# Optimization experiments

Hardware: AMD Instinct MI355X
Metric: run time of the kernel (lower is better)

The kernel has to match this reference:

```python
import jax, jax.numpy as jnp
import numpy as np

D_MODEL = 2048
N_HEADS = 32
N_KV_HEADS = 8
ROPE_BASE = 10000.0


def setup_inputs() -> dict:
    key = jax.random.key(0)
    ks = jax.random.split(key, 5)
    b, s, d = 2, 2048, D_MODEL
    hd = d // N_HEADS
    scale = 0.02
    return {
        "x": jax.random.normal(ks[0], (b, s, d), jnp.float32),
        "wq": jax.random.normal(ks[1], (N_HEADS * hd, d), jnp.float32) * scale,
        "wk": jax.random.normal(ks[2], (N_KV_HEADS * hd, d), jnp.float32) * scale,
        "wv": jax.random.normal(ks[3], (N_KV_HEADS * hd, d), jnp.float32) * scale,
        "wo": jax.random.normal(ks[4], (d, N_HEADS * hd), jnp.float32) * scale,
    }


def _rope_cos_sin(seq_len, head_dim):
    # theta_j = base^(-2j/d); freqs[i, j] = i * theta_j; repeat-interleave x2 on last dim
    theta = 1.0 / (ROPE_BASE ** (jnp.arange(0, head_dim, 2, dtype=jnp.float32) / head_dim))
    freqs = jnp.arange(seq_len, dtype=jnp.float32)[:, None] * theta[None, :]  # [S, hd/2]
    cos = jnp.repeat(jnp.cos(freqs), 2, axis=-1)[None, :, None, :]  # [1, S, 1, hd]
    sin = jnp.repeat(jnp.sin(freqs), 2, axis=-1)[None, :, None, :]
    return cos, sin


def _rotate(t):
    # interleaved rotate-half: (x0, x1, x2, x3, ...) -> (-x1, x0, -x3, x2, ...)
    t1 = t[..., ::2]
    t2 = t[..., 1::2]
    return jnp.stack([-t2, t1], axis=-1).reshape(t.shape)


def reference(x, wq, wk, wv, wo):
    b, s, d = x.shape
    hd = d // N_HEADS
    n_rep = N_HEADS // N_KV_HEADS

    q = (x @ wq.T).reshape(b, s, N_HEADS, hd)       # [b, s, H, hd]
    k = (x @ wk.T).reshape(b, s, N_KV_HEADS, hd)    # [b, s, G, hd]
    v = (x @ wv.T).reshape(b, s, N_KV_HEADS, hd)

    cos, sin = _rope_cos_sin(s, hd)
    q = q * cos + _rotate(q) * sin
    k = k * cos + _rotate(k) * sin

    # GQA without physical KV replication: group query heads by shared KV head.
    # repeat_interleave(n_rep, dim=2) maps kv head g -> query heads [g*n_rep, (g+1)*n_rep)
    qg = q.reshape(b, s, N_KV_HEADS, n_rep, hd)
    scale = 1.0 / jnp.sqrt(jnp.asarray(hd, q.dtype))
    scores = jnp.einsum('bqgrd,bkgd->bgrqk', qg, k) * scale  # [b, G, rep, Sq, Sk]

    causal = jnp.tril(jnp.ones((s, s), dtype=bool))
    scores = jnp.where(causal[None, None, None], scores, jnp.asarray(-jnp.inf, scores.dtype))
    attn = jax.nn.softmax(scores, axis=-1)

    out = jnp.einsum('bgrqk,bkgd->bqgrd', attn, v).reshape(b, s, N_HEADS * hd)
    return out @ wo.T
```

## Files before the change

### kernel.cpp

```cpp
#include <hip/hip_runtime.h>

typedef unsigned short u16;
typedef __attribute__((ext_vector_type(8))) short bf16x8;
typedef __attribute__((ext_vector_type(4))) float f32x4;

#define LOG2E 1.44269504088896340736f

__device__ inline u16 f2b(float f) {
    unsigned int u = __builtin_bit_cast(unsigned int, f);
    unsigned int r = u + 0x7fffu + ((u >> 16) & 1u);
    return (u16)(r >> 16);
}
__device__ inline float b2f(u16 h) {
    unsigned int u = ((unsigned int)h) << 16;
    return __builtin_bit_cast(float, u);
}

#define GLOAD_LDS16(g, l) \
    __builtin_amdgcn_global_load_lds( \
        (const __attribute__((address_space(1))) unsigned int*)(g), \
        (__attribute__((address_space(3))) unsigned int*)(l), 16, 0, 0)

__global__ __launch_bounds__(256) void cast_all(
    const float* __restrict__ x, const float* __restrict__ wq,
    const float* __restrict__ wk, const float* __restrict__ wv,
    const float* __restrict__ wo, u16* __restrict__ xb,
    u16* __restrict__ wqkvb, u16* __restrict__ wob) {
    long i = ((long)blockIdx.x * 256 + threadIdx.x) * 8;
    const float* s;
    u16* d;
    if (i < 8388608)       { s = x  + i;              d = xb + i; }
    else if (i < 12582912) { s = wq + (i - 8388608);  d = wqkvb + (i - 8388608); }
    else if (i < 13631488) { s = wk + (i - 12582912); d = wqkvb + 4194304 + (i - 12582912); }
    else if (i < 14680064) { s = wv + (i - 13631488); d = wqkvb + 5242880 + (i - 13631488); }
    else                   { s = wo + (i - 14680064); d = wob + (i - 14680064); }
    float4 v0 = *(const float4*)s;
    float4 v1 = *(const float4*)(s + 4);
    ushort4 o0 = make_ushort4(f2b(v0.x), f2b(v0.y), f2b(v0.z), f2b(v0.w));
    ushort4 o1 = make_ushort4(f2b(v1.x), f2b(v1.y), f2b(v1.z), f2b(v1.w));
    *(ushort4*)d = o0;
    *(ushort4*)(d + 4) = o1;
}

__global__ __launch_bounds__(256) void rope_vtrans(
    u16* __restrict__ qkv, u16* __restrict__ VT, float qscale) {
    const int S = 2048, RS = 3072;
    int tid = threadIdx.x;
    if (blockIdx.x < 5120) {
        int idx = blockIdx.x * 256 + tid;
        int row = idx / 320;
        int rem = idx - row * 320;
        int head = rem >> 3, chunk = rem & 7;
        int pos = row & 2047;
        int coloff;
        float scale;
        if (head < 32) { coloff = head * 64;               scale = qscale; }
        else           { coloff = 2048 + (head - 32) * 64; scale = 1.0f; }
        u16* p = qkv + (size_t)row * RS + coloff + chunk * 8;
        bf16x8 v = *(bf16x8*)p;
        float t0 = exp2f((float)(chunk * 4) * -0.41524101186092f);
        const float tc[4] = {1.0f, 0.74989420933246f, 0.56234132519035f, 0.42169650342858f};
        float fpos = (float)pos;
        #pragma unroll
        for (int i = 0; i < 4; i++) {
            float f = fpos * (t0 * tc[i]);
            float rev = f * 0.15915494309189535f;
            rev = rev - floorf(rev);
            float sn = __builtin_amdgcn_sinf(rev);
            float cs = __builtin_amdgcn_cosf(rev);
            float e0 = b2f((u16)v[2 * i]), e1 = b2f((u16)v[2 * i + 1]);
            v[2 * i]     = (short)f2b((e0 * cs - e1 * sn) * scale);
            v[2 * i + 1] = (short)f2b((e1 * cs + e0 * sn) * scale);
        }
        *(bf16x8*)p = v;
    } else {
        int bid = blockIdx.x - 5120;
        int st = bid & 31, g = (bid >> 5) & 7, b = bid >> 8;
        __shared__ u16 T[64 * 72];
        for (int c = tid; c < 512; c += 256) {
            int sr = c >> 3, dc = (c & 7) * 8;
            *(bf16x8*)&T[sr * 72 + dc] =
                *(const bf16x8*)(qkv + ((size_t)b * S + st * 64 + sr) * RS + 2560 + g * 64 + dc);
        }
        __syncthreads();
        for (int c = tid; c < 512; c += 256) {
            int d = c >> 3, sc = (c & 7) * 8;
            bf16x8 o;
            #pragma unroll
            for (int j = 0; j < 8; j++) o[j] = (short)T[(sc + j) * 72 + d];
            *(bf16x8*)(VT + ((size_t)((b * 8 + g) * 64 + d)) * S + st * 64 + sc) = o;
        }
    }
}

__global__ __launch_bounds__(256) void gemm_bt128(
    const u16* __restrict__ A, const u16* __restrict__ B, void* __restrict__ Cv,
    int M, int N, int K, int c_is_f32) {
    __shared__ u16 As[128 * 32];
    __shared__ u16 Bs[128 * 32];
    const int tid = threadIdx.x;
    const int lane = tid & 63, wave = tid >> 6;
    const int ln = lane & 15, quad = lane >> 4;
    const int wm = wave >> 1, wn = wave & 1;

    const int gx = gridDim.x;
    const int nwg = gx * gridDim.y;
    const int bid = blockIdx.y * gx + blockIdx.x;
    const int cpx = nwg >> 3;
    const int swz = (bid & 7) * cpx + (bid >> 3);
    const int m0 = (swz / gx) * 128, n0 = (swz % gx) * 128;

    const int srow = wave * 16 + (lane >> 2);
    const int skc = (lane & 3) * 8;
    const u16* Ag = A + (size_t)(m0 + srow) * K + skc;
    const u16* Bg = B + (size_t)(n0 + srow) * K + skc;

    f32x4 acc[4][4] = {};
    for (int k0 = 0; k0 < K; k0 += 32) {
        #pragma unroll
        for (int t = 0; t < 2; t++) {
            GLOAD_LDS16(Ag + (size_t)t * 64 * K + k0, As + t * 2048 + wave * 512);
            GLOAD_LDS16(Bg + (size_t)t * 64 * K + k0, Bs + t * 2048 + wave * 512);
        }
        __syncthreads();

        bf16x8 af[4], bfr[4];
        #pragma unroll
        for (int i = 0; i < 4; i++) {
            af[i]  = *(const bf16x8*)&As[(wm * 64 + i * 16 + ln) * 32 + quad * 8];
            bfr[i] = *(const bf16x8*)&Bs[(wn * 64 + i * 16 + ln) * 32 + quad * 8];
        }
        #pragma unroll
        for (int mi = 0; mi < 4; mi++)
            #pragma unroll
            for (int nt = 0; nt < 4; nt++)
                acc[mi][nt] = __builtin_amdgcn_mfma_f32_16x16x32_bf16(
                    af[mi], bfr[nt], acc[mi][nt], 0, 0, 0);
        __syncthreads();
    }

    #pragma unroll
    for (int mi = 0; mi < 4; mi++)
        #pragma unroll
        for (int nt = 0; nt < 4; nt++)
            #pragma unroll
            for (int r = 0; r < 4; r++) {
                int row = m0 + wm * 64 + mi * 16 + quad * 4 + r;
                int col = n0 + wn * 64 + nt * 16 + ln;
                float v = acc[mi][nt][r];
                if (c_is_f32) ((float*)Cv)[(size_t)row * N + col] = v;
                else          ((u16*)Cv)[(size_t)row * N + col] = f2b(v);
            }
}

__global__ __launch_bounds__(256) void attn_kernel(
    const u16* __restrict__ QKV, const u16* __restrict__ VT, u16* __restrict__ O) {
    const int S = 2048, RS = 3072, DO = 2048;
    const int b = blockIdx.z, h = blockIdx.y, p = blockIdx.x;
    const int g = h >> 2;
    const int qtl = p, qth = (S / 64 - 1) - p;
    const int tid = threadIdx.x;
    const int lane = tid & 63, wave = tid >> 6;
    const int ln = lane & 15, quad = lane >> 4;

    __shared__ u16 Ks[2][64 * 72];
    __shared__ u16 Psh[64 * 68];
    __shared__ u16 Psl[64 * 68];

    const u16* Qb = QKV + (size_t)b * S * RS + h * 64 + quad * 8;
    bf16x8 aqh0 = *(const bf16x8*)(Qb + (size_t)(qth * 64 + wave * 16 + ln) * RS);
    bf16x8 aqh1 = *(const bf16x8*)(Qb + (size_t)(qth * 64 + wave * 16 + ln) * RS + 32);
    bf16x8 aql0 = *(const bf16x8*)(Qb + (size_t)(qtl * 64 + wave * 16 + ln) * RS);
    bf16x8 aql1 = *(const bf16x8*)(Qb + (size_t)(qtl * 64 + wave * 16 + ln) * RS + 32);

    const u16* Kb = QKV + (size_t)b * S * RS + 2048 + g * 64;
    const u16* VTb = VT + (size_t)(b * 8 + g) * 64 * S;

    const bf16x8 vones = {0x3F80, 0x3F80, 0x3F80, 0x3F80, 0x3F80, 0x3F80, 0x3F80, 0x3F80};

    f32x4 acch[5] = {}, accl[5] = {};

    const int r0 = tid >> 3;
    const int dc0 = (tid & 7) * 8;
    bf16x8 kreg0, kreg1;
    bf16x8 vr[2][4];
    auto loadK = [&](int kt) {
        kreg0 = *(const bf16x8*)(Kb + (size_t)(kt * 64 + r0) * RS + dc0);
        kreg1 = *(const bf16x8*)(Kb + (size_t)(kt * 64 + r0 + 32) * RS + dc0);
    };
    auto loadV = [&](int kt) {
        #pragma unroll
        for (int kk = 0; kk < 2; kk++)
            #pragma unroll
            for (int nt = 0; nt < 4; nt++)
                vr[kk][nt] = *(const bf16x8*)(VTb + (size_t)(nt * 16 + ln) * S
                                              + kt * 64 + kk * 32 + quad * 8);
    };

    auto body = [&](int kt, bool DUAL, bool MH, bool ML) {
        u16* KsC = &Ks[kt & 1][0];
        u16* KsN = &Ks[(kt & 1) ^ 1][0];
        if (kt < qth) {
            *(bf16x8*)&KsN[r0 * 72 + dc0] = kreg0;
            *(bf16x8*)&KsN[(r0 + 32) * 72 + dc0] = kreg1;
        }
        if (kt + 2 <= qth) loadK(kt + 2);

        f32x4 sh[4] = {}, sl[4] = {};
        __builtin_amdgcn_s_setprio(1);
        #pragma unroll
        for (int nt = 0; nt < 4; nt++) {
            bf16x8 bk0 = *(const bf16x8*)&KsC[(nt * 16 + ln) * 72 + quad * 8];
            bf16x8 bk1 = *(const bf16x8*)&KsC[(nt * 16 + ln) * 72 + 32 + quad * 8];
            sh[nt] = __builtin_amdgcn_mfma_f32_16x16x32_bf16(aqh0, bk0, sh[nt], 0, 0, 0);
            sh[nt] = __builtin_amdgcn_mfma_f32_16x16x32_bf16(aqh1, bk1, sh[nt], 0, 0, 0);
            if (DUAL) {
                sl[nt] = __builtin_amdgcn_mfma_f32_16x16x32_bf16(aql0, bk0, sl[nt], 0, 0, 0);
                sl[nt] = __builtin_amdgcn_mfma_f32_16x16x32_bf16(aql1, bk1, sl[nt], 0, 0, 0);
            }
        }
        __builtin_amdgcn_s_setprio(0);

        if (MH) {
            #pragma unroll
            for (int nt = 0; nt < 4; nt++)
                #pragma unroll
                for (int r = 0; r < 4; r++)
                    if (nt * 16 + ln > wave * 16 + quad * 4 + r) sh[nt][r] = -INFINITY;
        }
        #pragma unroll
        for (int nt = 0; nt < 4; nt++)
            #pragma unroll
            for (int r = 0; r < 4; r++) {
                float pv = exp2f(sh[nt][r]);
                Psh[(wave * 16 + quad * 4 + r) * 68 + nt * 16 + ln] =
                    (u16)(__builtin_bit_cast(unsigned int, pv) >> 16);
            }
        if (DUAL) {
            if (ML) {
                #pragma unroll
                for (int nt = 0; nt < 4; nt++)
                    #pragma unroll
                    for (int r = 0; r < 4; r++)
                        if (nt * 16 + ln > wave * 16 + quad * 4 + r) sl[nt][r] = -INFINITY;
            }
            #pragma unroll
            for (int nt = 0; nt < 4; nt++)
                #pragma unroll
                for (int r = 0; r < 4; r++) {
                    float pv = exp2f(sl[nt][r]);
                    Psl[(wave * 16 + quad * 4 + r) * 68 + nt * 16 + ln] =
                        (u16)(__builtin_bit_cast(unsigned int, pv) >> 16);
                }
        }

        __builtin_amdgcn_s_setprio(1);
        #pragma unroll
        for (int kk = 0; kk < 2; kk++) {
            bf16x8 aph = *(const bf16x8*)&Psh[(wave * 16 + ln) * 68 + kk * 32 + quad * 8];
            #pragma unroll
            for (int nt = 0; nt < 4; nt++)
                acch[nt] = __builtin_amdgcn_mfma_f32_16x16x32_bf16(aph, vr[kk][nt], acch[nt], 0, 0, 0);
            acch[4] = __builtin_amdgcn_mfma_f32_16x16x32_bf16(aph, vones, acch[4], 0, 0, 0);
            if (DUAL) {
                bf16x8 apl = *(const bf16x8*)&Psl[(wave * 16 + ln) * 68 + kk * 32 + quad * 8];
                #pragma unroll
                for (int nt = 0; nt < 4; nt++)
                    accl[nt] = __builtin_amdgcn_mfma_f32_16x16x32_bf16(apl, vr[kk][nt], accl[nt], 0, 0, 0);
                accl[4] = __builtin_amdgcn_mfma_f32_16x16x32_bf16(apl, vones, accl[4], 0, 0, 0);
            }
        }
        __builtin_amdgcn_s_setprio(0);

        if (kt < qth) loadV(kt + 1);
        __syncthreads();
    };

    loadK(0);
    loadV(0);
    *(bf16x8*)&Ks[0][r0 * 72 + dc0] = kreg0;
    *(bf16x8*)&Ks[0][(r0 + 32) * 72 + dc0] = kreg1;
    loadK(1);
    __syncthreads();

    for (int kt = 0; kt < qtl; kt++) body(kt, true, false, false);
    body(qtl, true, false, true);
    for (int kt = qtl + 1; kt < qth; kt++) body(kt, false, false, false);
    body(qth, false, true, false);

    u16* Ob = O + (size_t)b * S * DO + h * 64;
    #pragma unroll
    for (int r = 0; r < 4; r++) {
        float invh = 1.0f / acch[4][r];
        float invl = 1.0f / accl[4][r];
        int qh = qth * 64 + wave * 16 + quad * 4 + r;
        int ql = qtl * 64 + wave * 16 + quad * 4 + r;
        #pragma unroll
        for (int nt = 0; nt < 4; nt++) {
            Ob[(size_t)qh * DO + nt * 16 + ln] = f2b(acch[nt][r] * invh);
            Ob[(size_t)ql * DO + nt * 16 + ln] = f2b(accl[nt][r] * invl);
        }
    }
}

extern "C" void kernel_launch(void* const* d_in, const int* in_sizes, int n_in,
                              void* d_out, int out_size, void* d_ws, size_t ws_size,
                              hipStream_t stream) {
    const float* x  = (const float*)d_in[0];
    const float* wq = (const float*)d_in[1];
    const float* wk = (const float*)d_in[2];
    const float* wv = (const float*)d_in[3];
    const float* wo = (const float*)d_in[4];

    const int B = 2, S = 2048, D = 2048, H = 32, KVH = 8;
    const int M = B * S;
    const int NQKV = 3072;

    char* ws = (char*)d_ws;
    size_t off = 0;
    auto alloc = [&](size_t bytes) {
        void* p = ws + off;
        off += (bytes + 255) & ~(size_t)255;
        return p;
    };
    u16* xb    = (u16*)alloc((size_t)M * D * 2);
    u16* wqkvb = (u16*)alloc((size_t)NQKV * D * 2);
    u16* wob   = (u16*)alloc((size_t)D * D * 2);
    u16* QKV   = (u16*)alloc((size_t)M * NQKV * 2);
    u16* AO = xb;
    u16* VT = wqkvb;

    cast_all<<<dim3(9216), 256, 0, stream>>>(x, wq, wk, wv, wo, xb, wqkvb, wob);

    gemm_bt128<<<dim3(NQKV / 128, M / 128), 256, 0, stream>>>(xb, wqkvb, QKV, M, NQKV, D, 0);

    const float sscale = 0.125f * LOG2E;
    rope_vtrans<<<dim3(5632), 256, 0, stream>>>(QKV, VT, sscale);

    attn_kernel<<<dim3(S / 128, H, B), 256, 0, stream>>>(QKV, VT, AO);

    gemm_bt128<<<dim3(D / 128, M / 128), 256, 0, stream>>>(AO, wob, d_out, M, D, D, 1);
}
```

Before: 375.9 us.

## Share K tiles across two query heads per block with XOR-swizzled LDS

The attention kernel now runs 512 threads per block, covering two query heads that share one KV head, so each K tile staged in LDS serves both heads and each thread loads one K vector instead of two. The K LDS layout drops its padding and uses an XOR swizzle to avoid bank conflicts, and the block index is remapped so neighbouring blocks land on different XCDs. The aim is to halve K global/LDS staging traffic per head and improve cache locality. The trade-off is larger blocks and register pressure under launch bounds of 512, which may lower occupancy. V fragments are still loaded per wave straight from global memory.

Result: no change. 372.9 us (-0.8%).

```diff
diff --git a/kernel.cpp b/kernel.cpp
--- a/kernel.cpp
+++ b/kernel.cpp
@@ -153,25 +153,30 @@
             }
 }
 
-__global__ __launch_bounds__(256) void attn_kernel(
+__global__ __launch_bounds__(512) void attn_kernel(
     const u16* __restrict__ QKV, const u16* __restrict__ VT, u16* __restrict__ O) {
     const int S = 2048, RS = 3072, DO = 2048;
-    const int b = blockIdx.z, h = blockIdx.y, p = blockIdx.x;
-    const int g = h >> 2;
-    const int qtl = p, qth = (S / 64 - 1) - p;
+    const int bid = blockIdx.x;
+    const int swz = (bid & 7) * 64 + (bid >> 3);
+    const int p = swz & 15, hp = (swz >> 4) & 15, b = swz >> 8;
+    const int g = hp >> 1;
+    const int qtl = p, qth = 31 - p;
     const int tid = threadIdx.x;
     const int lane = tid & 63, wave = tid >> 6;
+    const int hw = wave >> 2, lw = wave & 3;
+    const int h = hp * 2 + hw;
     const int ln = lane & 15, quad = lane >> 4;
 
-    __shared__ u16 Ks[2][64 * 72];
-    __shared__ u16 Psh[64 * 68];
-    __shared__ u16 Psl[64 * 68];
+    __shared__ u16 Ks[2][64 * 64];
+    __shared__ u16 Ps[4][64 * 68];
+    u16* Psh = &Ps[hw * 2 + 0][0];
+    u16* Psl = &Ps[hw * 2 + 1][0];
 
     const u16* Qb = QKV + (size_t)b * S * RS + h * 64 + quad * 8;
-    bf16x8 aqh0 = *(const bf16x8*)(Qb + (size_t)(qth * 64 + wave * 16 + ln) * RS);
-    bf16x8 aqh1 = *(const bf16x8*)(Qb + (size_t)(qth * 64 + wave * 16 + ln) * RS + 32);
-    bf16x8 aql0 = *(const bf16x8*)(Qb + (size_t)(qtl * 64 + wave * 16 + ln) * RS);
-    bf16x8 aql1 = *(const bf16x8*)(Qb + (size_t)(qtl * 64 + wave * 16 + ln) * RS + 32);
+    bf16x8 aqh0 = *(const bf16x8*)(Qb + (size_t)(qth * 64 + lw * 16 + ln) * RS);
+    bf16x8 aqh1 = *(const bf16x8*)(Qb + (size_t)(qth * 64 + lw * 16 + ln) * RS + 32);
+    bf16x8 aql0 = *(const bf16x8*)(Qb + (size_t)(qtl * 64 + lw * 16 + ln) * RS);
+    bf16x8 aql1 = *(const bf16x8*)(Qb + (size_t)(qtl * 64 + lw * 16 + ln) * RS + 32);
 
     const u16* Kb = QKV + (size_t)b * S * RS + 2048 + g * 64;
     const u16* VTb = VT + (size_t)(b * 8 + g) * 64 * S;
@@ -180,13 +185,13 @@
 
     f32x4 acch[5] = {}, accl[5] = {};
 
-    const int r0 = tid >> 3;
-    const int dc0 = (tid & 7) * 8;
-    bf16x8 kreg0, kreg1;
+    const int kr = tid >> 3;
+    const int ks = tid & 7;
+    const int kswz = ((ks ^ (kr & 7)) * 8);
+    bf16x8 kreg;
     bf16x8 vr[2][4];
     auto loadK = [&](int kt) {
-        kreg0 = *(const bf16x8*)(Kb + (size_t)(kt * 64 + r0) * RS + dc0);
-        kreg1 = *(const bf16x8*)(Kb + (size_t)(kt * 64 + r0 + 32) * RS + dc0);
+        kreg = *(const bf16x8*)(Kb + (size_t)(kt * 64 + kr) * RS + ks * 8);
     };
     auto loadV = [&](int kt) {
         #pragma unroll
@@ -201,17 +206,17 @@
         u16* KsC = &Ks[kt & 1][0];
         u16* KsN = &Ks[(kt & 1) ^ 1][0];
         if (kt < qth) {
-            *(bf16x8*)&KsN[r0 * 72 + dc0] = kreg0;
-            *(bf16x8*)&KsN[(r0 + 32) * 72 + dc0] = kreg1;
+            *(bf16x8*)&KsN[kr * 64 + kswz] = kreg;
         }
         if (kt + 2 <= qth) loadK(kt + 2);
 
+        const int rsw = ln & 7;
         f32x4 sh[4] = {}, sl[4] = {};
         __builtin_amdgcn_s_setprio(1);
         #pragma unroll
         for (int nt = 0; nt < 4; nt++) {
-            bf16x8 bk0 = *(const bf16x8*)&KsC[(nt * 16 + ln) * 72 + quad * 8];
-            bf16x8 bk1 = *(const bf16x8*)&KsC[(nt * 16 + ln) * 72 + 32 + quad * 8];
+            bf16x8 bk0 = *(const bf16x8*)&KsC[(nt * 16 + ln) * 64 + ((quad ^ rsw) * 8)];
+            bf16x8 bk1 = *(const bf16x8*)&KsC[(nt * 16 + ln) * 64 + (((quad + 4) ^ rsw) * 8)];
             sh[nt] = __builtin_amdgcn_mfma_f32_16x16x32_bf16(aqh0, bk0, sh[nt], 0, 0, 0);
             sh[nt] = __builtin_amdgcn_mfma_f32_16x16x32_bf16(aqh1, bk1, sh[nt], 0, 0, 0);
             if (DUAL) {
@@ -226,14 +231,14 @@
             for (int nt = 0; nt < 4; nt++)
                 #pragma unroll
                 for (int r = 0; r < 4; r++)
-                    if (nt * 16 + ln > wave * 16 + quad * 4 + r) sh[nt][r] = -INFINITY;
+                    if (nt * 16 + ln > lw * 16 + quad * 4 + r) sh[nt][r] = -INFINITY;
         }
         #pragma unroll
         for (int nt = 0; nt < 4; nt++)
             #pragma unroll
             for (int r = 0; r < 4; r++) {
                 float pv = exp2f(sh[nt][r]);
-                Psh[(wave * 16 + quad * 4 + r) * 68 + nt * 16 + ln] =
+                Psh[(lw * 16 + quad * 4 + r) * 68 + nt * 16 + ln] =
                     (u16)(__builtin_bit_cast(unsigned int, pv) >> 16);
             }
         if (DUAL) {
@@ -242,14 +247,14 @@
                 for (int nt = 0; nt < 4; nt++)
                     #pragma unroll
                     for (int r = 0; r < 4; r++)
-                        if (nt * 16 + ln > wave * 16 + quad * 4 + r) sl[nt][r] = -INFINITY;
+                        if (nt * 16 + ln > lw * 16 + quad * 4 + r) sl[nt][r] = -INFINITY;
             }
             #pragma unroll
             for (int nt = 0; nt < 4; nt++)
                 #pragma unroll
                 for (int r = 0; r < 4; r++) {
                     float pv = exp2f(sl[nt][r]);
-                    Psl[(wave * 16 + quad * 4 + r) * 68 + nt * 16 + ln] =
+                    Psl[(lw * 16 + quad * 4 + r) * 68 + nt * 16 + ln] =
                         (u16)(__builtin_bit_cast(unsigned int, pv) >> 16);
                 }
         }
@@ -257,13 +262,13 @@
         __builtin_amdgcn_s_setprio(1);
         #pragma unroll
         for (int kk = 0; kk < 2; kk++) {
-            bf16x8 aph = *(const bf16x8*)&Psh[(wave * 16 + ln) * 68 + kk * 32 + quad * 8];
+            bf16x8 aph = *(const bf16x8*)&Psh[(lw * 16 + ln) * 68 + kk * 32 + quad * 8];
             #pragma unroll
             for (int nt = 0; nt < 4; nt++)
                 acch[nt] = __builtin_amdgcn_mfma_f32_16x16x32_bf16(aph, vr[kk][nt], acch[nt], 0, 0, 0);
             acch[4] = __builtin_amdgcn_mfma_f32_16x16x32_bf16(aph, vones, acch[4], 0, 0, 0);
             if (DUAL) {
-                bf16x8 apl = *(const bf16x8*)&Psl[(wave * 16 + ln) * 68 + kk * 32 + quad * 8];
+                bf16x8 apl = *(const bf16x8*)&Psl[(lw * 16 + ln) * 68 + kk * 32 + quad * 8];
                 #pragma unroll
                 for (int nt = 0; nt < 4; nt++)
                     accl[nt] = __builtin_amdgcn_mfma_f32_16x16x32_bf16(apl, vr[kk][nt], accl[nt], 0, 0, 0);
@@ -278,8 +283,7 @@
 
     loadK(0);
     loadV(0);
-    *(bf16x8*)&Ks[0][r0 * 72 + dc0] = kreg0;
-    *(bf16x8*)&Ks[0][(r0 + 32) * 72 + dc0] = kreg1;
+    *(bf16x8*)&Ks[0][kr * 64 + kswz] = kreg;
     loadK(1);
     __syncthreads();
 
@@ -293,8 +297,8 @@
     for (int r = 0; r < 4; r++) {
         float invh = 1.0f / acch[4][r];
         float invl = 1.0f / accl[4][r];
-        int qh = qth * 64 + wave * 16 + quad * 4 + r;
-        int ql = qtl * 64 + wave * 16 + quad * 4 + r;
+        int qh = qth * 64 + lw * 16 + quad * 4 + r;
+        int ql = qtl * 64 + lw * 16 + quad * 4 + r;
         #pragma unroll
         for (int nt = 0; nt < 4; nt++) {
             Ob[(size_t)qh * DO + nt * 16 + ln] = f2b(acch[nt][r] * invh);
@@ -337,7 +341,7 @@
     const float sscale = 0.125f * LOG2E;
     rope_vtrans<<<dim3(5632), 256, 0, stream>>>(QKV, VT, sscale);
 
-    attn_kernel<<<dim3(S / 128, H, B), 256, 0, stream>>>(QKV, VT, AO);
+    attn_kernel<<<dim3(512), 512, 0, stream>>>(QKV, VT, AO);
 
     gemm_bt128<<<dim3(D / 128, M / 128), 256, 0, stream>>>(AO, wob, d_out, M, D, D, 1);
 }
```
